# Optimization experiments

Hardware: AMD Instinct MI355X
Metric: run time of the kernel (lower is better)

Reference implementation:

```python
import jax, jax.numpy as jnp
import numpy as np

B, C, L = 8, 256, 4096
OC = C // 2  # out_channels default
EPS = 1e-5


def setup_inputs() -> dict:
    key = jax.random.key(0)
    ks = jax.random.split(key, 12)
    s_in = 1.0 / np.sqrt(C)   # conv1d default init scale (kaiming-uniform-ish)
    s_oc = 1.0 / np.sqrt(OC)
    return {
        "x": jax.random.normal(ks[0], (B, C, L), dtype=jnp.float32),
        "g_w": jax.random.uniform(ks[1], (OC, C), jnp.float32, -s_in, s_in),
        "g_b": jax.random.uniform(ks[2], (OC,), jnp.float32, -s_in, s_in),
        # theta/phi weights: nn.init.normal_(w, 0.02) -> mean 0.02, std 1
        "theta_w": 0.02 + jax.random.normal(ks[3], (OC, C), dtype=jnp.float32),
        "theta_b": jax.random.uniform(ks[4], (OC,), jnp.float32, -s_in, s_in),
        "phi_w": 0.02 + jax.random.normal(ks[5], (OC, C), dtype=jnp.float32),
        "phi_b": jax.random.uniform(ks[6], (OC,), jnp.float32, -s_in, s_in),
        "W_w": jax.random.uniform(ks[7], (C, OC), jnp.float32, -s_oc, s_oc),
        "W_b": jax.random.uniform(ks[8], (C,), jnp.float32, -s_oc, s_oc),
        # BN affine: init to zero in the original; use small random for a meaningful test
        "gamma": 0.1 * jax.random.normal(ks[9], (C,), dtype=jnp.float32),
        "beta": 0.1 * jax.random.normal(ks[10], (C,), dtype=jnp.float32),
    }


def reference(x, g_w, g_b, theta_w, theta_b, phi_w, phi_b, W_w, W_b, gamma, beta):
    # x: (b, c, l). 1x1 conv == per-position linear map over channels.
    g_x = jnp.einsum('oc,bcl->bol', g_w, x) + g_b[None, :, None]        # (b, oc, l)
    theta_x = jnp.einsum('oc,bcl->bol', theta_w, x) + theta_b[None, :, None]
    phi_x = jnp.einsum('oc,bcl->bol', phi_w, x) + phi_b[None, :, None]
    # f = theta^T phi : (b, l, l) quadratic score matrix (no softmax)
    f = jnp.einsum('bok,bom->bkm', theta_x, phi_x)
    N = f.shape[-1]
    # y = (f @ g^T) / N, returned in (b, oc, l) layout
    y = jnp.einsum('bkm,bom->bok', f, g_x) / N
    W_y = jnp.einsum('co,bol->bcl', W_w, y) + W_b[None, :, None]        # (b, c, l)
    # BatchNorm1d (training mode: batch statistics over (b, l), biased var)
    mean = jnp.mean(W_y, axis=(0, 2), keepdims=True)
    var = jnp.mean((W_y - mean) ** 2, axis=(0, 2), keepdims=True)
    W_y = (W_y - mean) * jax.lax.rsqrt(var + EPS)
    W_y = gamma[None, :, None] * W_y + beta[None, :, None]
    return W_y + x  # residual
```

## Files before the change

### kernel.cpp

```cpp
#include <hip/hip_runtime.h>
#include <hip/hip_bf16.h>

#define B_ 8
#define C_ 256
#define OC_ 128
#define L_ 4096
#define EPS_ 1e-5f
#define SPLITK 8

typedef unsigned short u16;
typedef __attribute__((ext_vector_type(4))) unsigned short u16x4;
typedef __attribute__((ext_vector_type(4))) float f32x4;
typedef __attribute__((ext_vector_type(8))) short bf16x8;

__device__ inline u16 f2bf(float f) {
  union { __hip_bfloat16 h; u16 u; } v;
  v.h = __float2bfloat16(f);
  return v.u;
}
__device__ inline float bf2f(u16 u) {
  union { float f; unsigned u; } v;
  v.u = ((unsigned)u) << 16;
  return v.f;
}

__device__ inline void gload_lds16(const void* g, void* lds) {
  __builtin_amdgcn_global_load_lds(
      (const __attribute__((address_space(1))) unsigned int*)g,
      (__attribute__((address_space(3))) unsigned int*)lds, 16, 0, 0);
}

__global__ __launch_bounds__(256) void k_cvt(const float* __restrict__ x,
                                             u16* __restrict__ Xb,
                                             u16* __restrict__ XbT,
                                             float* __restrict__ spartial) {
  __shared__ u16 T[64][73];
  __shared__ float P[64][17];
  const int b = blockIdx.z, c0 = blockIdx.y * 64, l0 = blockIdx.x * 64;
  const int tid = threadIdx.x;
#pragma unroll
  for (int it = 0; it < 4; ++it) {
    int idx = it * 256 + tid;
    int row = idx >> 4;
    int col = (idx & 15) << 2;
    size_t gi = ((size_t)(b * C_ + c0 + row)) * L_ + l0 + col;
    float4 v = *(const float4*)(x + gi);
    u16 u0 = f2bf(v.x), u1 = f2bf(v.y), u2 = f2bf(v.z), u3 = f2bf(v.w);
    u16x4 u = {u0, u1, u2, u3};
    *(u16x4*)(Xb + gi) = u;
    T[row][col] = u0; T[row][col + 1] = u1; T[row][col + 2] = u2; T[row][col + 3] = u3;
    P[row][idx & 15] = v.x + v.y + v.z + v.w;
  }
  __syncthreads();
  if (tid < 64) {
    float acc = 0.f;
#pragma unroll
    for (int j = 0; j < 16; j++) acc += P[tid][j];
    spartial[(size_t)blockIdx.x * (B_ * C_) + b * C_ + c0 + tid] = acc;
  }
#pragma unroll
  for (int it = 0; it < 4; ++it) {
    int idx = it * 256 + tid;
    int lrow = idx >> 4;
    int ccol = (idx & 15) << 2;
    u16x4 u = {T[ccol][lrow], T[ccol + 1][lrow], T[ccol + 2][lrow], T[ccol + 3][lrow]};
    *(u16x4*)(XbT + ((size_t)b * L_ + l0 + lrow) * C_ + c0 + ccol) = u;
  }
}

__global__ __launch_bounds__(256) void k_xxt(const u16* __restrict__ Xb,
                                             float* __restrict__ Spart) {
  const int b = blockIdx.z, split = blockIdx.y;
  const int ti = blockIdx.x >> 1, tj = blockIdx.x & 1;
  __shared__ u16 lds[2 * 128 * 64];
  const int tid = threadIdx.x, lane = tid & 63;
  const int wid = tid >> 6, wr = wid >> 1, wc = wid & 1;
  const u16* Arows = Xb + ((size_t)b * C_ + ti * 128) * L_;
  const u16* Brows = Xb + ((size_t)b * C_ + tj * 128) * L_;
  const int k0 = split * (L_ / SPLITK);
  f32x4 acc[4][4] = {};
  for (int kt = 0; kt < L_ / SPLITK; kt += 64) {
    __syncthreads();
#pragma unroll
    for (int ch = 0; ch < 4; ch++) {
      int d = ch * 4096 + tid * 16;
      int row = d >> 7;
      int kb = (d & 127) ^ ((row & 7) << 4);
      gload_lds16(Arows + (size_t)row * L_ + k0 + kt + (kb >> 1), (char*)lds + d);
      gload_lds16(Brows + (size_t)row * L_ + k0 + kt + (kb >> 1), (char*)lds + 16384 + d);
    }
    asm volatile("s_waitcnt vmcnt(0)" ::: "memory");
    __syncthreads();
#pragma unroll
    for (int ks = 0; ks < 2; ks++) {
      bf16x8 af[4], bfr[4];
#pragma unroll
      for (int m = 0; m < 4; m++) {
        int row = wr * 64 + m * 16 + (lane & 15);
        int kb = ((ks << 6) + ((lane >> 4) << 4)) ^ ((row & 7) << 4);
        af[m] = *(const bf16x8*)((const char*)lds + row * 128 + kb);
      }
#pragma unroll
      for (int n = 0; n < 4; n++) {
        int row = wc * 64 + n * 16 + (lane & 15);
        int kb = ((ks << 6) + ((lane >> 4) << 4)) ^ ((row & 7) << 4);
        bfr[n] = *(const bf16x8*)((const char*)lds + 16384 + row * 128 + kb);
      }
#pragma unroll
      for (int m = 0; m < 4; m++)
#pragma unroll
        for (int n = 0; n < 4; n++)
          acc[m][n] = __builtin_amdgcn_mfma_f32_16x16x32_bf16(af[m], bfr[n], acc[m][n], 0, 0, 0);
    }
  }
  float* Sp = Spart + ((size_t)split * B_ + b) * C_ * C_;
#pragma unroll
  for (int m = 0; m < 4; m++)
#pragma unroll
    for (int n = 0; n < 4; n++) {
      int r0 = ti * 128 + wr * 64 + m * 16 + ((lane >> 4) << 2);
      int c0 = tj * 128 + wc * 64 + n * 16 + (lane & 15);
#pragma unroll
      for (int r = 0; r < 4; r++)
        Sp[(size_t)(r0 + r) * C_ + c0] = acc[m][n][r];
    }
}

__global__ __launch_bounds__(256) void k_sreduce(const float* __restrict__ Spart,
                                                 const float* __restrict__ spartial,
                                                 const float* __restrict__ g_w,
                                                 float* __restrict__ S,
                                                 u16* __restrict__ Sb,
                                                 float* __restrict__ s,
                                                 float* __restrict__ gwT) {
  const int bid = blockIdx.x, tid = threadIdx.x;
  if (bid < (B_ * C_ * C_) / 256) {
    size_t idx = (size_t)bid * 256 + tid;
    float acc = 0.f;
    for (int sp = 0; sp < SPLITK; sp++) acc += Spart[(size_t)sp * B_ * C_ * C_ + idx];
    S[idx] = acc;
    Sb[idx] = f2bf(acc);
  } else if (bid < (B_ * C_ * C_) / 256 + (B_ * C_) / 256) {
    int idx2 = (bid - (B_ * C_ * C_) / 256) * 256 + tid;
    float acc = 0.f;
#pragma unroll 8
    for (int i = 0; i < 64; i++) acc += spartial[(size_t)i * (B_ * C_) + idx2];
    s[idx2] = acc;
  } else {
    int t = bid - ((B_ * C_ * C_) / 256 + (B_ * C_) / 256);
    int o = t * 8 + (tid & 7);
    int cbase = (tid >> 3) * 8;
#pragma unroll
    for (int k = 0; k < 8; k++) {
      int c = cbase + k;
      gwT[c * OC_ + o] = g_w[o * C_ + c];
    }
  }
}

__global__ __launch_bounds__(256) void k_mid1(const float* __restrict__ S,
                                              const float* __restrict__ s,
                                              const float* __restrict__ phi_w,
                                              const float* __restrict__ phi_b,
                                              const float* __restrict__ gwT,
                                              const float* __restrict__ g_b,
                                              float* __restrict__ MT) {
  const int b = blockIdx.x >> 5, ot = blockIdx.x & 31;
  const int tid = threadIdx.x;
  __shared__ float pw[4][257], t2[4][257], sl[256], ps_s[4], pb_s[4], redw[4][4];
  sl[tid] = s[b * C_ + tid];
#pragma unroll
  for (int r = 0; r < 4; r++) pw[r][tid] = phi_w[(ot * 4 + r) * C_ + tid];
  if (tid < 4) pb_s[tid] = phi_b[ot * 4 + tid];
  __syncthreads();
  float acc4[4] = {};
  const float* Sbr = S + (size_t)b * C_ * C_;
#pragma unroll 4
  for (int cp = 0; cp < C_; cp++) {
    float sv = Sbr[(size_t)cp * C_ + tid];
#pragma unroll
    for (int r = 0; r < 4; r++) acc4[r] += pw[r][cp] * sv;
  }
  const int lane = tid & 63, w = tid >> 6;
#pragma unroll
  for (int r = 0; r < 4; r++) {
    float v = pw[r][tid] * sl[tid];
#pragma unroll
    for (int off = 1; off < 64; off <<= 1) v += __shfl_xor(v, off, 64);
    if (lane == 0) redw[w][r] = v;
  }
#pragma unroll
  for (int r = 0; r < 4; r++) t2[r][tid] = acc4[r] + pb_s[r] * sl[tid];
  __syncthreads();
  if (tid < 4) ps_s[tid] = redw[0][tid] + redw[1][tid] + redw[2][tid] + redw[3][tid];
  __syncthreads();
  const int o = tid & 127, half = tid >> 7;
  float m0 = 0.f, m1 = 0.f;
#pragma unroll 4
  for (int c = 0; c < C_; c++) {
    float gv = gwT[c * OC_ + o];
    m0 += t2[half * 2][c] * gv;
    m1 += t2[half * 2 + 1][c] * gv;
  }
  float gb = g_b[o];
  int r0 = half * 2;
  MT[((size_t)b * OC_ + o) * OC_ + ot * 4 + r0]     = m0 + (ps_s[r0] + (float)L_ * pb_s[r0]) * gb;
  MT[((size_t)b * OC_ + o) * OC_ + ot * 4 + r0 + 1] = m1 + (ps_s[r0 + 1] + (float)L_ * pb_s[r0 + 1]) * gb;
}

__global__ __launch_bounds__(256) void k_mid2(const float* __restrict__ MT,
                                              const float* __restrict__ W_w,
                                              const float* __restrict__ theta_w,
                                              const float* __restrict__ theta_b,
                                              const float* __restrict__ W_b,
                                              const float* __restrict__ s,
                                              u16* __restrict__ Qb,
                                              float* __restrict__ qv,
                                              float* __restrict__ qs_g,
                                              float* __restrict__ sum1) {
  const int b = blockIdx.x >> 6, ct = blockIdx.x & 63;
  const int c0 = ct * 4;
  const int tid = threadIdx.x;
  __shared__ float ww[4][OC_], u_s[4][OC_ + 2], s_l[C_], q_s[4], redq[4][4];
  s_l[tid] = s[b * C_ + tid];
#pragma unroll
  for (int i = tid; i < 4 * OC_; i += 256)
    ww[i >> 7][i & 127] = W_w[(c0 + (i >> 7)) * OC_ + (i & 127)];
  __syncthreads();
  const int op = tid & 127, rh = tid >> 7;
  float ua0 = 0.f, ua1 = 0.f;
  const float* MTb = MT + (size_t)b * OC_ * OC_;
#pragma unroll 4
  for (int o = 0; o < OC_; o++) {
    float mv = MTb[(size_t)o * OC_ + op];
    ua0 += ww[rh * 2][o] * mv;
    ua1 += ww[rh * 2 + 1][o] * mv;
  }
  u_s[rh * 2][op] = ua0 * (1.f / (float)L_);
  u_s[rh * 2 + 1][op] = ua1 * (1.f / (float)L_);
  __syncthreads();
  {
    const int r = tid >> 6, lane = tid & 63;
    float v = u_s[r][lane] * theta_b[lane] + u_s[r][lane + 64] * theta_b[lane + 64];
#pragma unroll
    for (int off = 1; off < 64; off <<= 1) v += __shfl_xor(v, off, 64);
    if (lane == 0) {
      float qval = v + W_b[c0 + r];
      q_s[r] = qval;
      qv[b * C_ + c0 + r] = qval;
    }
  }
  float qa[4] = {};
#pragma unroll 2
  for (int o = 0; o < OC_; o++) {
    float tv = theta_w[(size_t)o * C_ + tid];
#pragma unroll
    for (int r = 0; r < 4; r++) qa[r] += u_s[r][o] * tv;
  }
#pragma unroll
  for (int r = 0; r < 4; r++)
    Qb[((size_t)b * C_ + c0 + r) * C_ + tid] = f2bf(qa[r]);
  const int lane = tid & 63, w = tid >> 6;
#pragma unroll
  for (int r = 0; r < 4; r++) {
    float v = qa[r] * s_l[tid];
#pragma unroll
    for (int off = 1; off < 64; off <<= 1) v += __shfl_xor(v, off, 64);
    if (lane == 0) redq[w][r] = v;
  }
  __syncthreads();
  if (tid < 4) {
    float qs = redq[0][tid] + redq[1][tid] + redq[2][tid] + redq[3][tid];
    qs_g[b * C_ + c0 + tid] = qs;
    sum1[b * C_ + c0 + tid] = qs + (float)L_ * q_s[tid];
  }
}

__global__ __launch_bounds__(256) void k_ystat(const u16* __restrict__ Qb,
                                               const u16* __restrict__ Sb,
                                               float* __restrict__ e2part) {
  const int chs = blockIdx.x, ct = blockIdx.y, b = blockIdx.z;
  __shared__ u16 lds[2 * 128 * 64];
  __shared__ float e2s[128][2];
  const int tid = threadIdx.x, lane = tid & 63;
  const int wid = tid >> 6, wr = wid >> 1, wc = wid & 1;
  const u16* Abase = Qb + ((size_t)b * C_ + ct * 128) * C_;
  const u16* Bbase = Sb + ((size_t)b * C_ + chs * 128) * C_;
  f32x4 acc[4][4] = {};
  for (int k0 = 0; k0 < C_; k0 += 64) {
    __syncthreads();
#pragma unroll
    for (int ch = 0; ch < 4; ch++) {
      int d = ch * 4096 + tid * 16;
      int row = d >> 7;
      int kb = (d & 127) ^ ((row & 7) << 4);
      gload_lds16(Abase + (size_t)row * C_ + k0 + (kb >> 1), (char*)lds + d);
      gload_lds16(Bbase + (size_t)row * C_ + k0 + (kb >> 1), (char*)lds + 16384 + d);
    }
    asm volatile("s_waitcnt vmcnt(0)" ::: "memory");
    __syncthreads();
#pragma unroll
    for (int ks = 0; ks < 2; ks++) {
      bf16x8 af[4], bfr[4];
#pragma unroll
      for (int m = 0; m < 4; m++) {
        int row = wr * 64 + m * 16 + (lane & 15);
        int kb = ((ks << 6) + ((lane >> 4) << 4)) ^ ((row & 7) << 4);
        af[m] = *(const bf16x8*)((const char*)lds + row * 128 + kb);
      }
#pragma unroll
      for (int n = 0; n < 4; n++) {
        int row = wc * 64 + n * 16 + (lane & 15);
        int kb = ((ks << 6) + ((lane >> 4) << 4)) ^ ((row & 7) << 4);
        bfr[n] = *(const bf16x8*)((const char*)lds + 16384 + row * 128 + kb);
      }
#pragma unroll
      for (int m = 0; m < 4; m++)
#pragma unroll
        for (int n = 0; n < 4; n++)
          acc[m][n] = __builtin_amdgcn_mfma_f32_16x16x32_bf16(af[m], bfr[n], acc[m][n], 0, 0, 0);
    }
  }
  float e2a[4][4];
#pragma unroll
  for (int m = 0; m < 4; m++)
#pragma unroll
    for (int r = 0; r < 4; r++) e2a[m][r] = 0.f;
#pragma unroll
  for (int m = 0; m < 4; m++)
#pragma unroll
    for (int n = 0; n < 4; n++) {
      int ch = chs * 128 + wc * 64 + n * 16 + (lane & 15);
#pragma unroll
      for (int r = 0; r < 4; r++) {
        int c_loc = wr * 64 + m * 16 + ((lane >> 4) << 2) + r;
        float q2 = bf2f(Qb[((size_t)b * C_ + ct * 128 + c_loc) * C_ + ch]);
        e2a[m][r] += acc[m][n][r] * q2;
      }
    }
#pragma unroll
  for (int m = 0; m < 4; m++)
#pragma unroll
    for (int r = 0; r < 4; r++) {
      float v = e2a[m][r];
      v += __shfl_xor(v, 1, 64);
      v += __shfl_xor(v, 2, 64);
      v += __shfl_xor(v, 4, 64);
      v += __shfl_xor(v, 8, 64);
      if ((lane & 15) == 0) {
        int c_loc = wr * 64 + m * 16 + ((lane >> 4) << 2) + r;
        e2s[c_loc][wc] = v;
      }
    }
  __syncthreads();
  if (tid < 128)
    e2part[((size_t)chs * B_ + b) * C_ + ct * 128 + tid] = e2s[tid][0] + e2s[tid][1];
}

__global__ __launch_bounds__(256) void k_out(const u16* __restrict__ Qb,
                                             const float* __restrict__ qv,
                                             const float* __restrict__ qs_g,
                                             const float* __restrict__ sum1,
                                             const float* __restrict__ e2part,
                                             const float* __restrict__ gamma,
                                             const float* __restrict__ beta,
                                             const u16* __restrict__ XbT,
                                             const u16* __restrict__ Xb,
                                             float* __restrict__ out) {
  const int b = blockIdx.z, ct = blockIdx.y, lt = blockIdx.x;
  __shared__ u16 lds[2 * 128 * 64];
  __shared__ float gsc_s[128], qp_s[128];
  const int tid = threadIdx.x, lane = tid & 63;
  const int wid = tid >> 6, wr = wid >> 1, wc = wid & 1;
  if (tid < 128) {
    int c = ct * 128 + tid;
    float m = 0.f, e = 0.f;
#pragma unroll
    for (int bb = 0; bb < B_; bb++) {
      m += sum1[bb * C_ + c];
      float e2 = e2part[(size_t)bb * C_ + c] + e2part[((size_t)B_ + bb) * C_ + c];
      float qq = qv[bb * C_ + c];
      float qs = qs_g[bb * C_ + c];
      e += e2 + 2.f * qq * qs + (float)L_ * qq * qq;
    }
    const float inv_n = 1.f / (float)(B_ * L_);
    m *= inv_n;
    e *= inv_n;
    float var = e - m * m;
    float g = gamma[c] * rsqrtf(var + EPS_);
    gsc_s[tid] = g;
    qp_s[tid] = g * (qv[b * C_ + c] - m) + beta[c];
  }
  const u16* Abase = Qb + ((size_t)b * C_ + ct * 128) * C_;
  const u16* Bbase = XbT + ((size_t)b * L_ + lt * 128) * C_;
  f32x4 acc[4][4] = {};
  for (int k0 = 0; k0 < C_; k0 += 64) {
    __syncthreads();
#pragma unroll
    for (int ch = 0; ch < 4; ch++) {
      int d = ch * 4096 + tid * 16;
      int row = d >> 7;
      int kb = (d & 127) ^ ((row & 7) << 4);
      gload_lds16(Abase + (size_t)row * C_ + k0 + (kb >> 1), (char*)lds + d);
      gload_lds16(Bbase + (size_t)row * C_ + k0 + (kb >> 1), (char*)lds + 16384 + d);
    }
    asm volatile("s_waitcnt vmcnt(0)" ::: "memory");
    __syncthreads();
#pragma unroll
    for (int ks = 0; ks < 2; ks++) {
      bf16x8 af[4], bfr[4];
#pragma unroll
      for (int m = 0; m < 4; m++) {
        int row = wr * 64 + m * 16 + (lane & 15);
        int kb = ((ks << 6) + ((lane >> 4) << 4)) ^ ((row & 7) << 4);
        af[m] = *(const bf16x8*)((const char*)lds + row * 128 + kb);
      }
#pragma unroll
      for (int n = 0; n < 4; n++) {
        int row = wc * 64 + n * 16 + (lane & 15);
        int kb = ((ks << 6) + ((lane >> 4) << 4)) ^ ((row & 7) << 4);
        bfr[n] = *(const bf16x8*)((const char*)lds + 16384 + row * 128 + kb);
      }
#pragma unroll
      for (int m = 0; m < 4; m++)
#pragma unroll
        for (int n = 0; n < 4; n++)
          acc[m][n] = __builtin_amdgcn_mfma_f32_16x16x32_bf16(af[m], bfr[n], acc[m][n], 0, 0, 0);
    }
  }
#pragma unroll
  for (int m = 0; m < 4; m++)
#pragma unroll
    for (int n = 0; n < 4; n++) {
      int cl = wr * 64 + m * 16 + ((lane >> 4) << 2);
      int c = ct * 128 + cl;
      int l = lt * 128 + wc * 64 + n * 16 + (lane & 15);
#pragma unroll
      for (int r = 0; r < 4; r++) {
        size_t gi = ((size_t)b * C_ + c + r) * L_ + l;
        out[gi] = gsc_s[cl + r] * acc[m][n][r] + bf2f(Xb[gi]) + qp_s[cl + r];
      }
    }
}

extern "C" void kernel_launch(void* const* d_in, const int* in_sizes, int n_in,
                              void* d_out, int out_size, void* d_ws, size_t ws_size,
                              hipStream_t stream) {
  const float* x       = (const float*)d_in[0];
  const float* g_w     = (const float*)d_in[1];
  const float* g_b     = (const float*)d_in[2];
  const float* theta_w = (const float*)d_in[3];
  const float* theta_b = (const float*)d_in[4];
  const float* phi_w   = (const float*)d_in[5];
  const float* phi_b   = (const float*)d_in[6];
  const float* W_w     = (const float*)d_in[7];
  const float* W_b     = (const float*)d_in[8];
  const float* gamma   = (const float*)d_in[9];
  const float* beta    = (const float*)d_in[10];
  float* out = (float*)d_out;

  float* ws = (float*)d_ws;
  size_t off = 0;
  float* Spart    = ws + off; off += (size_t)SPLITK * B_ * C_ * C_;
  float* S        = ws + off; off += (size_t)B_ * C_ * C_;
  float* spartial = ws + off; off += (size_t)B_ * C_ * 64;
  float* s_       = ws + off; off += B_ * C_;
  float* gwT      = ws + off; off += C_ * OC_;
  float* MT       = ws + off; off += (size_t)B_ * OC_ * OC_;
  float* qv       = ws + off; off += B_ * C_;
  float* qs_g     = ws + off; off += B_ * C_;
  float* sum1     = ws + off; off += B_ * C_;
  float* e2part   = ws + off; off += 2 * B_ * C_;
  u16* Sb  = (u16*)(ws + off); off += (size_t)B_ * C_ * C_ / 2;
  u16* Qb  = (u16*)(ws + off); off += (size_t)B_ * C_ * C_ / 2;
  u16* Xb  = (u16*)(ws + off); off += (size_t)B_ * C_ * L_ / 2;
  u16* XbT = (u16*)(ws + off); off += (size_t)B_ * C_ * L_ / 2;

  k_cvt<<<dim3(L_ / 64, C_ / 64, B_), 256, 0, stream>>>(x, Xb, XbT, spartial);
  k_xxt<<<dim3(4, SPLITK, B_), 256, 0, stream>>>(Xb, Spart);
  k_sreduce<<<(B_ * C_ * C_) / 256 + (B_ * C_) / 256 + 16, 256, 0, stream>>>(
      Spart, spartial, g_w, S, Sb, s_, gwT);
  k_mid1<<<B_ * 32, 256, 0, stream>>>(S, s_, phi_w, phi_b, gwT, g_b, MT);
  k_mid2<<<B_ * 64, 256, 0, stream>>>(MT, W_w, theta_w, theta_b, W_b, s_,
                                      Qb, qv, qs_g, sum1);
  k_ystat<<<dim3(2, 2, B_), 256, 0, stream>>>(Qb, Sb, e2part);
  k_out<<<dim3(L_ / 128, C_ / 128, B_), 256, 0, stream>>>(
      Qb, qv, qs_g, sum1, e2part, gamma, beta, XbT, Xb, out);
}
```

Before: 133.2 us.

## Shrink XX^T tiles, split-K ystat, add BN finalize kernel, double-buffer GEMMs

k_xxt now uses 64x64 tiles with double-buffered LDS staging, so it launches 4x more blocks and overlaps global loads with MFMA work. k_ystat is split along K into four slices, growing its grid from 32 to 128 blocks, and writes eight partial e2 sums per channel instead of two. The per-block BatchNorm statistic recomputation in k_out moves into a small new k_fin kernel, and k_out's K loop is double-buffered too. The goal is better GPU occupancy and load/compute overlap. The cost is an extra kernel launch, more partial-sum traffic, and twice the LDS per block in k_out.

```diff
diff --git a/kernel.cpp b/kernel.cpp
--- a/kernel.cpp
+++ b/kernel.cpp
@@ -71,55 +71,64 @@
 __global__ __launch_bounds__(256) void k_xxt(const u16* __restrict__ Xb,
                                              float* __restrict__ Spart) {
   const int b = blockIdx.z, split = blockIdx.y;
-  const int ti = blockIdx.x >> 1, tj = blockIdx.x & 1;
-  __shared__ u16 lds[2 * 128 * 64];
+  const int ti = blockIdx.x >> 2, tj = blockIdx.x & 3;
+  __shared__ u16 lds[2][2][64 * 64];
   const int tid = threadIdx.x, lane = tid & 63;
   const int wid = tid >> 6, wr = wid >> 1, wc = wid & 1;
-  const u16* Arows = Xb + ((size_t)b * C_ + ti * 128) * L_;
-  const u16* Brows = Xb + ((size_t)b * C_ + tj * 128) * L_;
+  const u16* Arows = Xb + ((size_t)b * C_ + ti * 64) * L_;
+  const u16* Brows = Xb + ((size_t)b * C_ + tj * 64) * L_;
   const int k0 = split * (L_ / SPLITK);
-  f32x4 acc[4][4] = {};
-  for (int kt = 0; kt < L_ / SPLITK; kt += 64) {
-    __syncthreads();
-#pragma unroll
-    for (int ch = 0; ch < 4; ch++) {
+  f32x4 acc[2][2] = {};
+
+  auto STAGE = [&](int buf, int kt) {
+#pragma unroll
+    for (int ch = 0; ch < 2; ch++) {
       int d = ch * 4096 + tid * 16;
       int row = d >> 7;
       int kb = (d & 127) ^ ((row & 7) << 4);
-      gload_lds16(Arows + (size_t)row * L_ + k0 + kt + (kb >> 1), (char*)lds + d);
-      gload_lds16(Brows + (size_t)row * L_ + k0 + kt + (kb >> 1), (char*)lds + 16384 + d);
+      gload_lds16(Arows + (size_t)row * L_ + k0 + kt + (kb >> 1), (char*)lds[buf][0] + d);
+      gload_lds16(Brows + (size_t)row * L_ + k0 + kt + (kb >> 1), (char*)lds[buf][1] + d);
+    }
+  };
+
+  STAGE(0, 0);
+  asm volatile("s_waitcnt vmcnt(0)" ::: "memory");
+  __syncthreads();
+  int cur = 0;
+  for (int kt = 0; kt < L_ / SPLITK; kt += 64) {
+    if (kt + 64 < L_ / SPLITK) STAGE(cur ^ 1, kt + 64);
+#pragma unroll
+    for (int kk = 0; kk < 2; kk++) {
+      bf16x8 af[2], bfr[2];
+#pragma unroll
+      for (int m = 0; m < 2; m++) {
+        int row = wr * 32 + m * 16 + (lane & 15);
+        int kb = ((kk << 6) + ((lane >> 4) << 4)) ^ ((row & 7) << 4);
+        af[m] = *(const bf16x8*)((const char*)lds[cur][0] + row * 128 + kb);
+      }
+#pragma unroll
+      for (int n = 0; n < 2; n++) {
+        int row = wc * 32 + n * 16 + (lane & 15);
+        int kb = ((kk << 6) + ((lane >> 4) << 4)) ^ ((row & 7) << 4);
+        bfr[n] = *(const bf16x8*)((const char*)lds[cur][1] + row * 128 + kb);
+      }
+#pragma unroll
+      for (int m = 0; m < 2; m++)
+#pragma unroll
+        for (int n = 0; n < 2; n++)
+          acc[m][n] = __builtin_amdgcn_mfma_f32_16x16x32_bf16(af[m], bfr[n], acc[m][n], 0, 0, 0);
     }
     asm volatile("s_waitcnt vmcnt(0)" ::: "memory");
     __syncthreads();
-#pragma unroll
-    for (int ks = 0; ks < 2; ks++) {
-      bf16x8 af[4], bfr[4];
-#pragma unroll
-      for (int m = 0; m < 4; m++) {
-        int row = wr * 64 + m * 16 + (lane & 15);
-        int kb = ((ks << 6) + ((lane >> 4) << 4)) ^ ((row & 7) << 4);
-        af[m] = *(const bf16x8*)((const char*)lds + row * 128 + kb);
-      }
-#pragma unroll
-      for (int n = 0; n < 4; n++) {
-        int row = wc * 64 + n * 16 + (lane & 15);
-        int kb = ((ks << 6) + ((lane >> 4) << 4)) ^ ((row & 7) << 4);
-        bfr[n] = *(const bf16x8*)((const char*)lds + 16384 + row * 128 + kb);
-      }
-#pragma unroll
-      for (int m = 0; m < 4; m++)
-#pragma unroll
-        for (int n = 0; n < 4; n++)
-          acc[m][n] = __builtin_amdgcn_mfma_f32_16x16x32_bf16(af[m], bfr[n], acc[m][n], 0, 0, 0);
-    }
+    cur ^= 1;
   }
   float* Sp = Spart + ((size_t)split * B_ + b) * C_ * C_;
 #pragma unroll
-  for (int m = 0; m < 4; m++)
-#pragma unroll
-    for (int n = 0; n < 4; n++) {
-      int r0 = ti * 128 + wr * 64 + m * 16 + ((lane >> 4) << 2);
-      int c0 = tj * 128 + wc * 64 + n * 16 + (lane & 15);
+  for (int m = 0; m < 2; m++)
+#pragma unroll
+    for (int n = 0; n < 2; n++) {
+      int r0 = ti * 64 + wr * 32 + m * 16 + ((lane >> 4) << 2);
+      int c0 = tj * 64 + wc * 32 + n * 16 + (lane & 15);
 #pragma unroll
       for (int r = 0; r < 4; r++)
         Sp[(size_t)(r0 + r) * C_ + c0] = acc[m][n][r];
@@ -279,47 +288,47 @@
 __global__ __launch_bounds__(256) void k_ystat(const u16* __restrict__ Qb,
                                                const u16* __restrict__ Sb,
                                                float* __restrict__ e2part) {
-  const int chs = blockIdx.x, ct = blockIdx.y, b = blockIdx.z;
+  const int b = blockIdx.z;
+  const int chs = blockIdx.y >> 1, ct = blockIdx.y & 1;
+  const int ks = blockIdx.x;
   __shared__ u16 lds[2 * 128 * 64];
   __shared__ float e2s[128][2];
   const int tid = threadIdx.x, lane = tid & 63;
   const int wid = tid >> 6, wr = wid >> 1, wc = wid & 1;
   const u16* Abase = Qb + ((size_t)b * C_ + ct * 128) * C_;
   const u16* Bbase = Sb + ((size_t)b * C_ + chs * 128) * C_;
+  const int k0 = ks * 64;
   f32x4 acc[4][4] = {};
-  for (int k0 = 0; k0 < C_; k0 += 64) {
-    __syncthreads();
-#pragma unroll
-    for (int ch = 0; ch < 4; ch++) {
-      int d = ch * 4096 + tid * 16;
-      int row = d >> 7;
-      int kb = (d & 127) ^ ((row & 7) << 4);
-      gload_lds16(Abase + (size_t)row * C_ + k0 + (kb >> 1), (char*)lds + d);
-      gload_lds16(Bbase + (size_t)row * C_ + k0 + (kb >> 1), (char*)lds + 16384 + d);
-    }
-    asm volatile("s_waitcnt vmcnt(0)" ::: "memory");
-    __syncthreads();
-#pragma unroll
-    for (int ks = 0; ks < 2; ks++) {
-      bf16x8 af[4], bfr[4];
-#pragma unroll
-      for (int m = 0; m < 4; m++) {
-        int row = wr * 64 + m * 16 + (lane & 15);
-        int kb = ((ks << 6) + ((lane >> 4) << 4)) ^ ((row & 7) << 4);
-        af[m] = *(const bf16x8*)((const char*)lds + row * 128 + kb);
-      }
-#pragma unroll
-      for (int n = 0; n < 4; n++) {
-        int row = wc * 64 + n * 16 + (lane & 15);
-        int kb = ((ks << 6) + ((lane >> 4) << 4)) ^ ((row & 7) << 4);
-        bfr[n] = *(const bf16x8*)((const char*)lds + 16384 + row * 128 + kb);
-      }
-#pragma unroll
-      for (int m = 0; m < 4; m++)
-#pragma unroll
-        for (int n = 0; n < 4; n++)
-          acc[m][n] = __builtin_amdgcn_mfma_f32_16x16x32_bf16(af[m], bfr[n], acc[m][n], 0, 0, 0);
-    }
+#pragma unroll
+  for (int ch = 0; ch < 4; ch++) {
+    int d = ch * 4096 + tid * 16;
+    int row = d >> 7;
+    int kb = (d & 127) ^ ((row & 7) << 4);
+    gload_lds16(Abase + (size_t)row * C_ + k0 + (kb >> 1), (char*)lds + d);
+    gload_lds16(Bbase + (size_t)row * C_ + k0 + (kb >> 1), (char*)lds + 16384 + d);
+  }
+  asm volatile("s_waitcnt vmcnt(0)" ::: "memory");
+  __syncthreads();
+#pragma unroll
+  for (int kk = 0; kk < 2; kk++) {
+    bf16x8 af[4], bfr[4];
+#pragma unroll
+    for (int m = 0; m < 4; m++) {
+      int row = wr * 64 + m * 16 + (lane & 15);
+      int kb = ((kk << 6) + ((lane >> 4) << 4)) ^ ((row & 7) << 4);
+      af[m] = *(const bf16x8*)((const char*)lds + row * 128 + kb);
+    }
+#pragma unroll
+    for (int n = 0; n < 4; n++) {
+      int row = wc * 64 + n * 16 + (lane & 15);
+      int kb = ((kk << 6) + ((lane >> 4) << 4)) ^ ((row & 7) << 4);
+      bfr[n] = *(const bf16x8*)((const char*)lds + 16384 + row * 128 + kb);
+    }
+#pragma unroll
+    for (int m = 0; m < 4; m++)
+#pragma unroll
+      for (int n = 0; n < 4; n++)
+        acc[m][n] = __builtin_amdgcn_mfma_f32_16x16x32_bf16(af[m], bfr[n], acc[m][n], 0, 0, 0);
   }
   float e2a[4][4];
 #pragma unroll
@@ -354,79 +363,96 @@
     }
   __syncthreads();
   if (tid < 128)
-    e2part[((size_t)chs * B_ + b) * C_ + ct * 128 + tid] = e2s[tid][0] + e2s[tid][1];
-}
-
-__global__ __launch_bounds__(256) void k_out(const u16* __restrict__ Qb,
+    e2part[(((size_t)chs * 4 + ks) * B_ + b) * C_ + ct * 128 + tid] =
+        e2s[tid][0] + e2s[tid][1];
+}
+
+__global__ __launch_bounds__(256) void k_fin(const float* __restrict__ sum1,
+                                             const float* __restrict__ e2part,
                                              const float* __restrict__ qv,
                                              const float* __restrict__ qs_g,
-                                             const float* __restrict__ sum1,
-                                             const float* __restrict__ e2part,
                                              const float* __restrict__ gamma,
                                              const float* __restrict__ beta,
+                                             float* __restrict__ gsc_g,
+                                             float* __restrict__ qp_g) {
+  const int b = blockIdx.x, c = threadIdx.x;
+  float m = 0.f, e = 0.f;
+#pragma unroll
+  for (int bb = 0; bb < B_; bb++) {
+    m += sum1[bb * C_ + c];
+    float e2 = 0.f;
+#pragma unroll
+    for (int sl = 0; sl < 8; sl++) e2 += e2part[((size_t)sl * B_ + bb) * C_ + c];
+    float qq = qv[bb * C_ + c], qs = qs_g[bb * C_ + c];
+    e += e2 + 2.f * qq * qs + (float)L_ * qq * qq;
+  }
+  const float inv_n = 1.f / (float)(B_ * L_);
+  m *= inv_n;
+  e *= inv_n;
+  float var = e - m * m;
+  float g = gamma[c] * rsqrtf(var + EPS_);
+  if (b == 0) gsc_g[c] = g;
+  qp_g[b * C_ + c] = g * (qv[b * C_ + c] - m) + beta[c];
+}
+
+__global__ __launch_bounds__(256) void k_out(const u16* __restrict__ Qb,
+                                             const float* __restrict__ gsc_g,
+                                             const float* __restrict__ qp_g,
                                              const u16* __restrict__ XbT,
                                              const u16* __restrict__ Xb,
                                              float* __restrict__ out) {
   const int b = blockIdx.z, ct = blockIdx.y, lt = blockIdx.x;
-  __shared__ u16 lds[2 * 128 * 64];
+  __shared__ u16 lds[2][2 * 128 * 64];
   __shared__ float gsc_s[128], qp_s[128];
   const int tid = threadIdx.x, lane = tid & 63;
   const int wid = tid >> 6, wr = wid >> 1, wc = wid & 1;
   if (tid < 128) {
-    int c = ct * 128 + tid;
-    float m = 0.f, e = 0.f;
-#pragma unroll
-    for (int bb = 0; bb < B_; bb++) {
-      m += sum1[bb * C_ + c];
-      float e2 = e2part[(size_t)bb * C_ + c] + e2part[((size_t)B_ + bb) * C_ + c];
-      float qq = qv[bb * C_ + c];
-      float qs = qs_g[bb * C_ + c];
-      e += e2 + 2.f * qq * qs + (float)L_ * qq * qq;
-    }
-    const float inv_n = 1.f / (float)(B_ * L_);
-    m *= inv_n;
-    e *= inv_n;
-    float var = e - m * m;
-    float g = gamma[c] * rsqrtf(var + EPS_);
-    gsc_s[tid] = g;
-    qp_s[tid] = g * (qv[b * C_ + c] - m) + beta[c];
+    gsc_s[tid] = gsc_g[ct * 128 + tid];
+    qp_s[tid] = qp_g[b * C_ + ct * 128 + tid];
   }
   const u16* Abase = Qb + ((size_t)b * C_ + ct * 128) * C_;
   const u16* Bbase = XbT + ((size_t)b * L_ + lt * 128) * C_;
   f32x4 acc[4][4] = {};
-  for (int k0 = 0; k0 < C_; k0 += 64) {
-    __syncthreads();
+  auto STAGE = [&](int buf, int k0) {
 #pragma unroll
     for (int ch = 0; ch < 4; ch++) {
       int d = ch * 4096 + tid * 16;
       int row = d >> 7;
       int kb = (d & 127) ^ ((row & 7) << 4);
-      gload_lds16(Abase + (size_t)row * C_ + k0 + (kb >> 1), (char*)lds + d);
-      gload_lds16(Bbase + (size_t)row * C_ + k0 + (kb >> 1), (char*)lds + 16384 + d);
+      gload_lds16(Abase + (size_t)row * C_ + k0 + (kb >> 1), (char*)lds[buf] + d);
+      gload_lds16(Bbase + (size_t)row * C_ + k0 + (kb >> 1), (char*)lds[buf] + 16384 + d);
+    }
+  };
+  STAGE(0, 0);
+  asm volatile("s_waitcnt vmcnt(0)" ::: "memory");
+  __syncthreads();
+  int cur = 0;
+  for (int k0 = 0; k0 < C_; k0 += 64) {
+    if (k0 + 64 < C_) STAGE(cur ^ 1, k0 + 64);
+#pragma unroll
+    for (int kk = 0; kk < 2; kk++) {
+      bf16x8 af[4], bfr[4];
+#pragma unroll
+      for (int m = 0; m < 4; m++) {
+        int row = wr * 64 + m * 16 + (lane & 15);
+        int kb = ((kk << 6) + ((lane >> 4) << 4)) ^ ((row & 7) << 4);
+        af[m] = *(const bf16x8*)((const char*)lds[cur] + row * 128 + kb);
+      }
+#pragma unroll
+      for (int n = 0; n < 4; n++) {
+        int row = wc * 64 + n * 16 + (lane & 15);
+        int kb = ((kk << 6) + ((lane >> 4) << 4)) ^ ((row & 7) << 4);
+        bfr[n] = *(const bf16x8*)((const char*)lds[cur] + 16384 + row * 128 + kb);
+      }
+#pragma unroll
+      for (int m = 0; m < 4; m++)
+#pragma unroll
+        for (int n = 0; n < 4; n++)
+          acc[m][n] = __builtin_amdgcn_mfma_f32_16x16x32_bf16(af[m], bfr[n], acc[m][n], 0, 0, 0);
     }
     asm volatile("s_waitcnt vmcnt(0)" ::: "memory");
     __syncthreads();
-#pragma unroll
-    for (int ks = 0; ks < 2; ks++) {
-      bf16x8 af[4], bfr[4];
-#pragma unroll
-      for (int m = 0; m < 4; m++) {
-        int row = wr * 64 + m * 16 + (lane & 15);
-        int kb = ((ks << 6) + ((lane >> 4) << 4)) ^ ((row & 7) << 4);
-        af[m] = *(const bf16x8*)((const char*)lds + row * 128 + kb);
-      }
-#pragma unroll
-      for (int n = 0; n < 4; n++) {
-        int row = wc * 64 + n * 16 + (lane & 15);
-        int kb = ((ks << 6) + ((lane >> 4) << 4)) ^ ((row & 7) << 4);
-        bfr[n] = *(const bf16x8*)((const char*)lds + 16384 + row * 128 + kb);
-      }
-#pragma unroll
-      for (int m = 0; m < 4; m++)
-#pragma unroll
-        for (int n = 0; n < 4; n++)
-          acc[m][n] = __builtin_amdgcn_mfma_f32_16x16x32_bf16(af[m], bfr[n], acc[m][n], 0, 0, 0);
-    }
+    cur ^= 1;
   }
 #pragma unroll
   for (int m = 0; m < 4; m++)
@@ -470,20 +496,23 @@
   float* qv       = ws + off; off += B_ * C_;
   float* qs_g     = ws + off; off += B_ * C_;
   float* sum1     = ws + off; off += B_ * C_;
-  float* e2part   = ws + off; off += 2 * B_ * C_;
+  float* e2part   = ws + off; off += 8 * B_ * C_;
+  float* gsc_g    = ws + off; off += C_;
+  float* qp_g     = ws + off; off += B_ * C_;
   u16* Sb  = (u16*)(ws + off); off += (size_t)B_ * C_ * C_ / 2;
   u16* Qb  = (u16*)(ws + off); off += (size_t)B_ * C_ * C_ / 2;
   u16* Xb  = (u16*)(ws + off); off += (size_t)B_ * C_ * L_ / 2;
   u16* XbT = (u16*)(ws + off); off += (size_t)B_ * C_ * L_ / 2;
 
   k_cvt<<<dim3(L_ / 64, C_ / 64, B_), 256, 0, stream>>>(x, Xb, XbT, spartial);
-  k_xxt<<<dim3(4, SPLITK, B_), 256, 0, stream>>>(Xb, Spart);
+  k_xxt<<<dim3(16, SPLITK, B_), 256, 0, stream>>>(Xb, Spart);
   k_sreduce<<<(B_ * C_ * C_) / 256 + (B_ * C_) / 256 + 16, 256, 0, stream>>>(
       Spart, spartial, g_w, S, Sb, s_, gwT);
   k_mid1<<<B_ * 32, 256, 0, stream>>>(S, s_, phi_w, phi_b, gwT, g_b, MT);
   k_mid2<<<B_ * 64, 256, 0, stream>>>(MT, W_w, theta_w, theta_b, W_b, s_,
                                       Qb, qv, qs_g, sum1);
-  k_ystat<<<dim3(2, 2, B_), 256, 0, stream>>>(Qb, Sb, e2part);
+  k_ystat<<<dim3(4, 4, B_), 256, 0, stream>>>(Qb, Sb, e2part);
+  k_fin<<<B_, 256, 0, stream>>>(sum1, e2part, qv, qs_g, gamma, beta, gsc_g, qp_g);
   k_out<<<dim3(L_ / 128, C_ / 128, B_), 256, 0, stream>>>(
-      Qb, qv, qs_g, sum1, e2part, gamma, beta, XbT, Xb, out);
-}
+      Qb, gsc_g, qp_g, XbT, Xb, out);
+}
```

Measured after the change: 126.7 us. -4.9%, faster.
